# Kernel optimization log

Measured on AMD Instinct MI355X. Metric: run time of the kernel, lower is better.

## Reference

```python
import jax, jax.numpy as jnp
import numpy as np

B, L, H, E, M = 4, 4096, 8, 64, 64
IN_CH, OUT_CH = 512, 512
SCALE = 1.0 / (IN_CH * OUT_CH)


def setup_inputs() -> dict:
    key = jax.random.key(0)
    k0, k1, k2, k3, k4 = jax.random.split(key, 5)
    q = jax.random.normal(k0, (B, L, H, E), dtype=jnp.float32)
    k = jax.random.normal(k1, (B, L, H, E), dtype=jnp.float32)
    v = jax.random.normal(k2, (B, L, H, E), dtype=jnp.float32)
    # torch.rand on a complex dtype fills real and imag parts with U[0,1)
    w_real = SCALE * jax.random.uniform(k3, (H, H, E, M), dtype=jnp.float32)
    w_imag = SCALE * jax.random.uniform(k4, (H, H, E, M), dtype=jnp.float32)
    # mode_select_method != 'random' -> lowest M modes, sorted
    index = jnp.arange(M, dtype=jnp.int32)
    mask = 0
    return {"q": q, "k": k, "v": v, "w_real": w_real, "w_imag": w_imag, "index": index, "mask": mask}


def reference(q, k, v, w_real, w_imag, index, mask):
    weights = w_real + 1j * w_imag                      # [H,H,E,M] complex64
    x = jnp.transpose(q, (0, 2, 3, 1))                   # [B,H,E,L]
    x_ft = jnp.fft.rfft(x, axis=-1)                      # [B,H,E,L//2+1]
    xg = jnp.take(x_ft, index, axis=-1)                  # gather selected modes: [B,H,E,M]
    # per-(E, mode) head-mixing: 'bix,iox->box' batched over modes
    res = jnp.einsum('bixm,ioxm->boxm', xg, weights)     # [B,H,E,M]
    Lh = L // 2 + 1
    out_ft = jnp.zeros((B, H, E, Lh), dtype=res.dtype).at[..., :M].set(res)
    x_out = jnp.fft.irfft(out_ft, n=L, axis=-1)          # [B,H,E,L] float32
    return x_out
```

## Files before the change

### kernel.cpp

```cpp
#include <hip/hip_runtime.h>

#define Bsz 4
#define Lsz 4096
#define HEsz 512
#define SPLIT 16

typedef __attribute__((ext_vector_type(8))) short short8;
typedef __attribute__((ext_vector_type(4))) float f32x4;

#define OFF_CF  0u
#define OFF_C1P (1u<<20)

static __device__ __forceinline__ unsigned short f2bf(float f) {
    union { float f; unsigned u; } v; v.f = f;
    unsigned u = v.u;
    return (unsigned short)((u + 0x7fffu + ((u >> 16) & 1u)) >> 16);
}
static __device__ __forceinline__ unsigned pk2(float a, float b) {
    return (unsigned)f2bf(a) | ((unsigned)f2bf(b) << 16);
}
static __device__ __forceinline__ float bf2f(unsigned short u) {
    union { unsigned u; float f; } v; v.u = ((unsigned)u) << 16;
    return v.f;
}
static __device__ __forceinline__ void sc(int m, int l, float* s, float* c) {
    int r = (m * l) & (Lsz - 1);
    float ang = (float)r * (6.283185307179586f / (float)Lsz);
    __sincosf(ang, s, c);
}

__global__ __launch_bounds__(256, 2) void k_dft(const float* __restrict__ q,
                                                unsigned short* __restrict__ C1P) {
    __shared__ unsigned short As[64 * 64];
    __shared__ unsigned short Bs[128 * 64];
    const int ks = blockIdx.x, ht = blockIdx.y, b = blockIdx.z;
    const int he0 = ht * 64;
    const int t = threadIdx.x, lane = t & 63, w = t >> 6;
    const int wtm = w & 1, wtn = w >> 1;
    const int quad = lane >> 4, lid = lane & 15;
    f32x4 acc[2][4] = {};

    const int kbeg = ks * (Lsz / SPLIT);
    const float* qp0 = q + ((size_t)(b * Lsz + kbeg + w * 16) * HEsz + he0 + lane);

    float f[16], f2[16];
#pragma unroll
    for (int j = 0; j < 16; ++j) f[j] = qp0[(size_t)j * HEsz];

#pragma unroll
    for (int ch = 0; ch < 4; ++ch) {
        {
            uint4 p0 = make_uint4(pk2(f[0], f[1]), pk2(f[2], f[3]), pk2(f[4], f[5]), pk2(f[6], f[7]));
            uint4 p1 = make_uint4(pk2(f[8], f[9]), pk2(f[10], f[11]), pk2(f[12], f[13]), pk2(f[14], f[15]));
            int row = lane;
            int cb0 = (w * 2) ^ (row & 7), cb1 = (w * 2 + 1) ^ (row & 7);
            *(uint4*)(As + row * 64 + cb0 * 8) = p0;
            *(uint4*)(As + row * 64 + cb1 * 8) = p1;
        }
        if (ch < 3) {
            const float* qp = qp0 + (size_t)(ch + 1) * 64 * HEsz;
#pragma unroll
            for (int j = 0; j < 16; ++j) f2[j] = qp[(size_t)j * HEsz];
        }
        {
            int m = t & 63, lg = t >> 6;
            int c0 = 2 * m, c1 = 2 * m + 1;
            const int l0 = kbeg + ch * 64;
#pragma unroll
            for (int h = 0; h < 2; ++h) {
                float sv[8], cv[8];
#pragma unroll
                for (int j = 0; j < 8; ++j)
                    sc(m, l0 + lg * 16 + h * 8 + j, &sv[j], &cv[j]);
                uint4 pc = make_uint4(pk2(cv[0], cv[1]), pk2(cv[2], cv[3]),
                                      pk2(cv[4], cv[5]), pk2(cv[6], cv[7]));
                uint4 ps = make_uint4(pk2(-sv[0], -sv[1]), pk2(-sv[2], -sv[3]),
                                      pk2(-sv[4], -sv[5]), pk2(-sv[6], -sv[7]));
                int lb = lg * 2 + h;
                *(uint4*)(Bs + c0 * 64 + ((lb ^ (c0 & 7)) * 8)) = pc;
                *(uint4*)(Bs + c1 * 64 + ((lb ^ (c1 & 7)) * 8)) = ps;
            }
        }
        __syncthreads();
#pragma unroll
        for (int kst = 0; kst < 2; ++kst) {
            short8 af[2], bfr[4];
#pragma unroll
            for (int mt = 0; mt < 2; ++mt) {
                int m = wtm * 32 + mt * 16 + lid;
                int cb = (kst * 4 + quad) ^ (m & 7);
                af[mt] = *(short8*)(As + m * 64 + cb * 8);
            }
#pragma unroll
            for (int nt = 0; nt < 4; ++nt) {
                int n = wtn * 64 + nt * 16 + lid;
                int cb = (kst * 4 + quad) ^ (n & 7);
                bfr[nt] = *(short8*)(Bs + n * 64 + cb * 8);
            }
#pragma unroll
            for (int mt = 0; mt < 2; ++mt)
#pragma unroll
                for (int nt = 0; nt < 4; ++nt)
                    acc[mt][nt] = __builtin_amdgcn_mfma_f32_16x16x32_bf16(af[mt], bfr[nt], acc[mt][nt], 0, 0, 0);
        }
        __syncthreads();
        if (ch < 3) {
#pragma unroll
            for (int j = 0; j < 16; ++j) f[j] = f2[j];
        }
    }
#pragma unroll
    for (int mt = 0; mt < 2; ++mt)
#pragma unroll
        for (int nt = 0; nt < 4; ++nt) {
            int col = wtn * 64 + nt * 16 + lid;
#pragma unroll
            for (int r = 0; r < 4; ++r) {
                int row = wtm * 32 + mt * 16 + quad * 4 + r;
                int cb = (col >> 3) ^ (row & 15);
                Bs[row * 128 + cb * 8 + (col & 7)] = f2bf(acc[mt][nt][r]);
            }
        }
    __syncthreads();
    unsigned short* dst = C1P + (((size_t)ks * Bsz + b) * HEsz + he0) * 128;
#pragma unroll
    for (int it = 0; it < 4; ++it) {
        int slot = t + it * 256;
        int r = slot >> 4, cb = slot & 15;
        *(uint4*)(dst + (size_t)r * 128 + cb * 8) =
            *(const uint4*)(Bs + r * 128 + ((cb ^ (r & 15)) * 8));
    }
}

__global__ __launch_bounds__(256) void k_mixreduce(const unsigned short* __restrict__ C1P,
                                                   const float* __restrict__ wr,
                                                   const float* __restrict__ wi,
                                                   unsigned short* __restrict__ Cf) {
    __shared__ float X[8][128];
    const int e = blockIdx.x & 63, b = blockIdx.x >> 6;
    const int t = threadIdx.x;
    const int i = t >> 5, c4 = t & 31;
    size_t off = ((size_t)b * HEsz + i * 64 + e) * 128 + c4 * 4;
    float sx = 0.f, sy = 0.f, sz = 0.f, sw = 0.f;
#pragma unroll
    for (int sp = 0; sp < SPLIT; ++sp) {
        uint2 v = *(const uint2*)(C1P + off + (size_t)sp * (Bsz * HEsz * 128));
        sx += bf2f((unsigned short)(v.x & 0xffff));
        sy += bf2f((unsigned short)(v.x >> 16));
        sz += bf2f((unsigned short)(v.y & 0xffff));
        sw += bf2f((unsigned short)(v.y >> 16));
    }
    *(float4*)&X[i][c4 * 4] = make_float4(sx, sy, sz, sw);
    __syncthreads();
#pragma unroll
    for (int it = 0; it < 2; ++it) {
        int item = t + it * 256;
        int o = item >> 6, m = item & 63;
        float ar = 0.f, ai = 0.f;
#pragma unroll
        for (int i2 = 0; i2 < 8; ++i2) {
            float xr = X[i2][2 * m], xi = X[i2][2 * m + 1];
            size_t wo = ((size_t)(i2 * 8 + o) * 64 + e) * 64 + m;
            float wrv = wr[wo], wiv = wi[wo];
            ar += xr * wrv - xi * wiv;
            ai += xr * wiv + xi * wrv;
        }
        int row = b * HEsz + o * 64 + e;
        *(unsigned*)(Cf + (size_t)row * 128 + 2 * m) = pk2(ar, -ai);
    }
}

__global__ __launch_bounds__(256, 2) void k_idft(const unsigned short* __restrict__ Cf,
                                                 float* __restrict__ out) {
    __shared__ unsigned short As[128 * 128];
    __shared__ unsigned short Bs[128 * 128];
    const int l0 = blockIdx.x * 128, row0 = blockIdx.y * 128;
    const int t = threadIdx.x, lane = t & 63, w = t >> 6;
    const int wtm = w & 1, wtn = w >> 1;
    const int quad = lane >> 4, lid = lane & 15;
    uint4 a[8];
#pragma unroll
    for (int it = 0; it < 8; ++it) {
        int slot = t + it * 256;
        int r = slot >> 4, cb = slot & 15;
        a[it] = *(const uint4*)(Cf + (size_t)(row0 + r) * 128 + cb * 8);
    }
    {
        int lr = t >> 1, half = t & 1;
        int lg = l0 + lr;
#pragma unroll
        for (int jj = 0; jj < 8; ++jj) {
            unsigned wv[4];
#pragma unroll
            for (int j = 0; j < 4; ++j) {
                int m = half * 32 + jj * 4 + j;
                float s, co; sc(m, lg, &s, &co);
                float wm = (m == 0) ? (1.0f / Lsz) : (2.0f / Lsz);
                wv[j] = pk2(wm * co, wm * s);
            }
            int cb = half * 8 + jj;
            *(uint4*)(Bs + lr * 128 + ((cb ^ (lr & 15)) * 8)) =
                make_uint4(wv[0], wv[1], wv[2], wv[3]);
        }
    }
#pragma unroll
    for (int it = 0; it < 8; ++it) {
        int slot = t + it * 256;
        int r = slot >> 4, cb = slot & 15;
        *(uint4*)(As + r * 128 + ((cb ^ (r & 15)) * 8)) = a[it];
    }
    __syncthreads();
    f32x4 acc[4][4] = {};
#pragma unroll
    for (int kst = 0; kst < 4; ++kst) {
        short8 af[4], bfr[4];
#pragma unroll
        for (int mt = 0; mt < 4; ++mt) {
            int m = wtm * 64 + mt * 16 + lid;
            int cb = (kst * 4 + quad) ^ (m & 15);
            af[mt] = *(short8*)(As + m * 128 + cb * 8);
        }
#pragma unroll
        for (int nt = 0; nt < 4; ++nt) {
            int n = wtn * 64 + nt * 16 + lid;
            int cb = (kst * 4 + quad) ^ (n & 15);
            bfr[nt] = *(short8*)(Bs + n * 128 + cb * 8);
        }
#pragma unroll
        for (int mt = 0; mt < 4; ++mt)
#pragma unroll
            for (int nt = 0; nt < 4; ++nt)
                acc[mt][nt] = __builtin_amdgcn_mfma_f32_16x16x32_bf16(af[mt], bfr[nt], acc[mt][nt], 0, 0, 0);
    }
    __syncthreads();
    float* outb = (float*)As;
#pragma unroll
    for (int mt = 0; mt < 4; ++mt)
#pragma unroll
        for (int nt = 0; nt < 4; ++nt) {
            int col = wtn * 64 + nt * 16 + lid;
            int c4 = col >> 2, cr = col & 3;
#pragma unroll
            for (int r = 0; r < 4; ++r) {
                int row = wtm * 64 + mt * 16 + quad * 4 + r;
                outb[(size_t)row * 128 + ((c4 ^ (row & 7)) << 2) + cr] = acc[mt][nt][r];
            }
        }
    __syncthreads();
#pragma unroll
    for (int it = 0; it < 16; ++it) {
        int slot = t + it * 256;
        int r = slot >> 5, c4 = slot & 31;
        float4 v = *(float4*)(outb + (size_t)r * 128 + ((c4 ^ (r & 7)) << 2));
        *(float4*)(out + (size_t)(row0 + r) * Lsz + l0 + c4 * 4) = v;
    }
}

extern "C" void kernel_launch(void* const* d_in, const int* in_sizes, int n_in,
                              void* d_out, int out_size, void* d_ws, size_t ws_size,
                              hipStream_t stream) {
    const float* q      = (const float*)d_in[0];
    const float* w_real = (const float*)d_in[3];
    const float* w_imag = (const float*)d_in[4];
    float* out = (float*)d_out;
    char* ws = (char*)d_ws;

    unsigned short* Cf  = (unsigned short*)(ws + OFF_CF);
    unsigned short* C1P = (unsigned short*)(ws + OFF_C1P);

    k_dft      <<<dim3(SPLIT, 8, 4), 256, 0, stream>>>(q, C1P);
    k_mixreduce<<<256, 256, 0, stream>>>(C1P, w_real, w_imag, Cf);
    k_idft     <<<dim3(32, 16), 256, 0, stream>>>(Cf, out);
}
```

Baseline: 144.3 us.

## Fuse DFT, mix-reduce and inverse DFT into one cooperative kernel with grid syncs

After: 253.9 us. 1.76x slower.

```diff
diff --git a/kernel.cpp b/kernel.cpp
--- a/kernel.cpp
+++ b/kernel.cpp
@@ -1,4 +1,7 @@
 #include <hip/hip_runtime.h>
+#include <hip/hip_cooperative_groups.h>
+
+namespace cg = cooperative_groups;
 
 #define Bsz 4
 #define Lsz 4096
@@ -27,6 +30,244 @@
     int r = (m * l) & (Lsz - 1);
     float ang = (float)r * (6.283185307179586f / (float)Lsz);
     __sincosf(ang, s, c);
+}
+
+__global__ __launch_bounds__(256, 2) void k_fused(const float* __restrict__ q,
+                                                  const float* __restrict__ wr,
+                                                  const float* __restrict__ wi,
+                                                  unsigned short* __restrict__ C1P,
+                                                  unsigned short* __restrict__ Cf,
+                                                  float* __restrict__ out) {
+    __shared__ unsigned short LDS[32768];
+    unsigned short* As1 = LDS;
+    unsigned short* Bs1 = LDS + 4096;
+    unsigned short* BI  = LDS + 16384;
+
+    const int bid = blockIdx.x;
+    const int t = threadIdx.x, lane = t & 63, w = t >> 6;
+    const int quad = lane >> 4, lid = lane & 15;
+
+    {
+        const int ks = bid & 15, ht = (bid >> 4) & 7, b = bid >> 7;
+        const int he0 = ht * 64;
+        const int wtm = w & 1, wtn = w >> 1;
+        f32x4 acc[2][4] = {};
+
+        const int kbeg = ks * (Lsz / SPLIT);
+        const float* qp0 = q + ((size_t)(b * Lsz + kbeg + w * 16) * HEsz + he0 + lane);
+
+        float f[16], f2[16];
+#pragma unroll
+        for (int j = 0; j < 16; ++j) f[j] = qp0[(size_t)j * HEsz];
+
+#pragma unroll
+        for (int ch = 0; ch < 4; ++ch) {
+            {
+                uint4 p0 = make_uint4(pk2(f[0], f[1]), pk2(f[2], f[3]), pk2(f[4], f[5]), pk2(f[6], f[7]));
+                uint4 p1 = make_uint4(pk2(f[8], f[9]), pk2(f[10], f[11]), pk2(f[12], f[13]), pk2(f[14], f[15]));
+                int row = lane;
+                int cb0 = (w * 2) ^ (row & 7), cb1 = (w * 2 + 1) ^ (row & 7);
+                *(uint4*)(As1 + row * 64 + cb0 * 8) = p0;
+                *(uint4*)(As1 + row * 64 + cb1 * 8) = p1;
+            }
+            if (ch < 3) {
+                const float* qp = qp0 + (size_t)(ch + 1) * 64 * HEsz;
+#pragma unroll
+                for (int j = 0; j < 16; ++j) f2[j] = qp[(size_t)j * HEsz];
+            }
+            {
+                int m = t & 63, lg = t >> 6;
+                int c0 = 2 * m, c1 = 2 * m + 1;
+                const int l0 = kbeg + ch * 64;
+#pragma unroll
+                for (int h = 0; h < 2; ++h) {
+                    float sv[8], cv[8];
+#pragma unroll
+                    for (int j = 0; j < 8; ++j)
+                        sc(m, l0 + lg * 16 + h * 8 + j, &sv[j], &cv[j]);
+                    uint4 pc = make_uint4(pk2(cv[0], cv[1]), pk2(cv[2], cv[3]),
+                                          pk2(cv[4], cv[5]), pk2(cv[6], cv[7]));
+                    uint4 ps = make_uint4(pk2(-sv[0], -sv[1]), pk2(-sv[2], -sv[3]),
+                                          pk2(-sv[4], -sv[5]), pk2(-sv[6], -sv[7]));
+                    int lb = lg * 2 + h;
+                    *(uint4*)(Bs1 + c0 * 64 + ((lb ^ (c0 & 7)) * 8)) = pc;
+                    *(uint4*)(Bs1 + c1 * 64 + ((lb ^ (c1 & 7)) * 8)) = ps;
+                }
+            }
+            __syncthreads();
+#pragma unroll
+            for (int kst = 0; kst < 2; ++kst) {
+                short8 af[2], bfr[4];
+#pragma unroll
+                for (int mt = 0; mt < 2; ++mt) {
+                    int m = wtm * 32 + mt * 16 + lid;
+                    int cb = (kst * 4 + quad) ^ (m & 7);
+                    af[mt] = *(short8*)(As1 + m * 64 + cb * 8);
+                }
+#pragma unroll
+                for (int nt = 0; nt < 4; ++nt) {
+                    int n = wtn * 64 + nt * 16 + lid;
+                    int cb = (kst * 4 + quad) ^ (n & 7);
+                    bfr[nt] = *(short8*)(Bs1 + n * 64 + cb * 8);
+                }
+#pragma unroll
+                for (int mt = 0; mt < 2; ++mt)
+#pragma unroll
+                    for (int nt = 0; nt < 4; ++nt)
+                        acc[mt][nt] = __builtin_amdgcn_mfma_f32_16x16x32_bf16(af[mt], bfr[nt], acc[mt][nt], 0, 0, 0);
+            }
+            __syncthreads();
+            if (ch < 3) {
+#pragma unroll
+                for (int j = 0; j < 16; ++j) f[j] = f2[j];
+            }
+        }
+#pragma unroll
+        for (int mt = 0; mt < 2; ++mt)
+#pragma unroll
+            for (int nt = 0; nt < 4; ++nt) {
+                int col = wtn * 64 + nt * 16 + lid;
+#pragma unroll
+                for (int r = 0; r < 4; ++r) {
+                    int row = wtm * 32 + mt * 16 + quad * 4 + r;
+                    int cb = (col >> 3) ^ (row & 15);
+                    Bs1[row * 128 + cb * 8 + (col & 7)] = f2bf(acc[mt][nt][r]);
+                }
+            }
+        __syncthreads();
+        unsigned short* dst = C1P + (((size_t)ks * Bsz + b) * HEsz + he0) * 128;
+#pragma unroll
+        for (int it = 0; it < 4; ++it) {
+            int slot = t + it * 256;
+            int r = slot >> 4, cb = slot & 15;
+            *(uint4*)(dst + (size_t)r * 128 + cb * 8) =
+                *(const uint4*)(Bs1 + r * 128 + ((cb ^ (r & 15)) * 8));
+        }
+    }
+
+    {
+        const int lt = bid & 31;
+        int lr = t >> 1, half = t & 1;
+        int lg = lt * 128 + lr;
+#pragma unroll
+        for (int jj = 0; jj < 8; ++jj) {
+            unsigned wv[4];
+#pragma unroll
+            for (int j = 0; j < 4; ++j) {
+                int m = half * 32 + jj * 4 + j;
+                float s, co; sc(m, lg, &s, &co);
+                float wm = (m == 0) ? (1.0f / Lsz) : (2.0f / Lsz);
+                wv[j] = pk2(wm * co, wm * s);
+            }
+            int cb = half * 8 + jj;
+            *(uint4*)(BI + lr * 128 + ((cb ^ (lr & 15)) * 8)) =
+                make_uint4(wv[0], wv[1], wv[2], wv[3]);
+        }
+    }
+
+    cg::this_grid().sync();
+
+    if (bid < 256) {
+        float* X = (float*)LDS;
+        const int e = bid & 63, b = bid >> 6;
+        const int i = t >> 5, c4 = t & 31;
+        size_t off = ((size_t)b * HEsz + i * 64 + e) * 128 + c4 * 4;
+        float sx = 0.f, sy = 0.f, sz = 0.f, sw = 0.f;
+#pragma unroll
+        for (int sp = 0; sp < SPLIT; ++sp) {
+            uint2 v = *(const uint2*)(C1P + off + (size_t)sp * (Bsz * HEsz * 128));
+            sx += bf2f((unsigned short)(v.x & 0xffff));
+            sy += bf2f((unsigned short)(v.x >> 16));
+            sz += bf2f((unsigned short)(v.y & 0xffff));
+            sw += bf2f((unsigned short)(v.y >> 16));
+        }
+        *(float4*)&X[(size_t)i * 128 + c4 * 4] = make_float4(sx, sy, sz, sw);
+        __syncthreads();
+#pragma unroll
+        for (int it = 0; it < 2; ++it) {
+            int item = t + it * 256;
+            int o = item >> 6, m = item & 63;
+            float ar = 0.f, ai = 0.f;
+#pragma unroll
+            for (int i2 = 0; i2 < 8; ++i2) {
+                float xr = X[(size_t)i2 * 128 + 2 * m], xi = X[(size_t)i2 * 128 + 2 * m + 1];
+                size_t wo = ((size_t)(i2 * 8 + o) * 64 + e) * 64 + m;
+                float wrv = wr[wo], wiv = wi[wo];
+                ar += xr * wrv - xi * wiv;
+                ai += xr * wiv + xi * wrv;
+            }
+            int row = b * HEsz + o * 64 + e;
+            *(unsigned*)(Cf + (size_t)row * 128 + 2 * m) = pk2(ar, -ai);
+        }
+    }
+
+    cg::this_grid().sync();
+
+    {
+        const int lt = bid & 31, rt = bid >> 5;
+        const int l0 = lt * 128, row0 = rt * 128;
+        const int wtm = w & 1, wtn = w >> 1;
+        unsigned short* As3 = LDS;
+
+        uint4 a[8];
+#pragma unroll
+        for (int it = 0; it < 8; ++it) {
+            int slot = t + it * 256;
+            int r = slot >> 4, cb = slot & 15;
+            a[it] = *(const uint4*)(Cf + (size_t)(row0 + r) * 128 + cb * 8);
+        }
+#pragma unroll
+        for (int it = 0; it < 8; ++it) {
+            int slot = t + it * 256;
+            int r = slot >> 4, cb = slot & 15;
+            *(uint4*)(As3 + r * 128 + ((cb ^ (r & 15)) * 8)) = a[it];
+        }
+        __syncthreads();
+        f32x4 acc[4][4] = {};
+#pragma unroll
+        for (int kst = 0; kst < 4; ++kst) {
+            short8 af[4], bfr[4];
+#pragma unroll
+            for (int mt = 0; mt < 4; ++mt) {
+                int m = wtm * 64 + mt * 16 + lid;
+                int cb = (kst * 4 + quad) ^ (m & 15);
+                af[mt] = *(short8*)(As3 + m * 128 + cb * 8);
+            }
+#pragma unroll
+            for (int nt = 0; nt < 4; ++nt) {
+                int n = wtn * 64 + nt * 16 + lid;
+                int cb = (kst * 4 + quad) ^ (n & 15);
+                bfr[nt] = *(short8*)(BI + n * 128 + cb * 8);
+            }
+#pragma unroll
+            for (int mt = 0; mt < 4; ++mt)
+#pragma unroll
+                for (int nt = 0; nt < 4; ++nt)
+                    acc[mt][nt] = __builtin_amdgcn_mfma_f32_16x16x32_bf16(af[mt], bfr[nt], acc[mt][nt], 0, 0, 0);
+        }
+        __syncthreads();
+        float* outb = (float*)LDS;
+#pragma unroll
+        for (int mt = 0; mt < 4; ++mt)
+#pragma unroll
+            for (int nt = 0; nt < 4; ++nt) {
+                int col = wtn * 64 + nt * 16 + lid;
+                int c4 = col >> 2, cr = col & 3;
+#pragma unroll
+                for (int r = 0; r < 4; ++r) {
+                    int row = wtm * 64 + mt * 16 + quad * 4 + r;
+                    outb[(size_t)row * 128 + ((c4 ^ (row & 7)) << 2) + cr] = acc[mt][nt][r];
+                }
+            }
+        __syncthreads();
+#pragma unroll
+        for (int it = 0; it < 16; ++it) {
+            int slot = t + it * 256;
+            int r = slot >> 5, c4 = slot & 31;
+            float4 v = *(float4*)(outb + (size_t)r * 128 + ((c4 ^ (r & 7)) << 2));
+            *(float4*)(out + (size_t)(row0 + r) * Lsz + l0 + c4 * 4) = v;
+        }
+    }
 }
 
 __global__ __launch_bounds__(256, 2) void k_dft(const float* __restrict__ q,
@@ -39,14 +280,11 @@
     const int wtm = w & 1, wtn = w >> 1;
     const int quad = lane >> 4, lid = lane & 15;
     f32x4 acc[2][4] = {};
-
     const int kbeg = ks * (Lsz / SPLIT);
     const float* qp0 = q + ((size_t)(b * Lsz + kbeg + w * 16) * HEsz + he0 + lane);
-
     float f[16], f2[16];
 #pragma unroll
     for (int j = 0; j < 16; ++j) f[j] = qp0[(size_t)j * HEsz];
-
 #pragma unroll
     for (int ch = 0; ch < 4; ++ch) {
         {
@@ -268,7 +506,13 @@
     unsigned short* Cf  = (unsigned short*)(ws + OFF_CF);
     unsigned short* C1P = (unsigned short*)(ws + OFF_C1P);
 
-    k_dft      <<<dim3(SPLIT, 8, 4), 256, 0, stream>>>(q, C1P);
-    k_mixreduce<<<256, 256, 0, stream>>>(C1P, w_real, w_imag, Cf);
-    k_idft     <<<dim3(32, 16), 256, 0, stream>>>(Cf, out);
-}
+    void* args[] = {(void*)&q, (void*)&w_real, (void*)&w_imag,
+                    (void*)&C1P, (void*)&Cf, (void*)&out};
+    hipError_t e = hipLaunchCooperativeKernel((const void*)k_fused, dim3(512), dim3(256),
+                                              args, 0, stream);
+    if (e != hipSuccess) {
+        k_dft      <<<dim3(SPLIT, 8, 4), 256, 0, stream>>>(q, C1P);
+        k_mixreduce<<<256, 256, 0, stream>>>(C1P, w_real, w_imag, Cf);
+        k_idft     <<<dim3(32, 16), 256, 0, stream>>>(Cf, out);
+    }
+}
```
